# Optimization experiments

Hardware: AMD Instinct MI355X
Metric: run time of the kernel (lower is better)

## Reference

```python
import jax, jax.numpy as jnp
import numpy as np

B, F_IN, F_OUT, D, K = 32, 64, 64, 512, 64


def setup_inputs() -> dict:
    key = jax.random.key(0)
    k1, k2, k3 = jax.random.split(key, 3)
    x = jax.random.normal(k1, (B, F_IN, D), dtype=jnp.float32)
    # Evaluated monomial-word operators: K matrices of size D x D
    word_ops = jax.random.normal(k2, (K, D, D), dtype=jnp.float32)
    # nn.init.uniform_ -> U[0,1)
    coeff = jax.random.uniform(k3, (F_OUT, F_IN, K), dtype=jnp.float32)
    return {"x": x, "word_ops": word_ops, "coeff": coeff}


def reference(x, word_ops, coeff):
    # Per sample in the torch code:
    #   evals[i, d, k] = (X @ W_k)[i, d] = sum_e X[i, e] * W[k, e, d]
    #   res = tensordot(coeff, evals, ([1, 2], [0, 2]))  -> [F_out, D]
    # Fully batched fused contraction (replaces the Python loop over batch):
    # evals: [B, F_in, D, K]
    evals = jnp.einsum('bie,ked->bidk', x, word_ops)
    # out: [B, F_out, D]
    out = jnp.einsum('oik,bidk->bod', coeff, evals)
    return out
```

## Files before the change

kernel.cpp:

```cpp
#include <hip/hip_runtime.h>


#define KK 32768

typedef __attribute__((ext_vector_type(8))) short bf16x8;
typedef __attribute__((ext_vector_type(4))) float f32x4;

__device__ __forceinline__ unsigned short f2bf(float f) {
  unsigned int u = __float_as_uint(f);
  return (unsigned short)((u + 0x7FFFu + ((u >> 16) & 1u)) >> 16);
}

__device__ __forceinline__ void gld16(void* lds, const void* g) {
  __builtin_amdgcn_global_load_lds((const __attribute__((address_space(1))) void*)g,
                                   (__attribute__((address_space(3))) void*)lds,
                                   16, 0, 0);
}

__global__ __launch_bounds__(256) void convW(const float* __restrict__ W,
                                             unsigned short* __restrict__ WbT) {
  __shared__ float tile[64][65];
  int bx = blockIdx.x;
  int k = bx >> 6, et = (bx >> 3) & 7, dt = bx & 7;
  int t = threadIdx.x;
  const float* src = W + ((size_t)k * 512 + (size_t)et * 64) * 512 + dt * 64;
  int rr = t >> 6, cc = t & 63;
#pragma unroll
  for (int p = 0; p < 16; p++) {
    int e = p * 4 + rr;
    tile[e][cc] = src[(size_t)e * 512 + cc];
  }
  __syncthreads();
  int dl = t >> 4, eg = t & 15;
#pragma unroll
  for (int p = 0; p < 4; p++) {
    int d = p * 16 + dl;
    ushort4 v;
    v.x = f2bf(tile[eg * 4 + 0][d]);
    v.y = f2bf(tile[eg * 4 + 1][d]);
    v.z = f2bf(tile[eg * 4 + 2][d]);
    v.w = f2bf(tile[eg * 4 + 3][d]);
    *(ushort4*)(WbT + (size_t)(dt * 64 + d) * KK + k * 512 + et * 64 + eg * 4) = v;
  }
}

__global__ __launch_bounds__(256) void convXC(const float* __restrict__ x,
                                              const float* __restrict__ c,
                                              unsigned short* __restrict__ xT,
                                              unsigned short* __restrict__ cb) {
  __shared__ unsigned short lds[64 * 130];
  int t = threadIdx.x;
  if (blockIdx.x < 128) {
    int bx = blockIdx.x;
    int b = bx >> 2, ec = bx & 3;
    const float* src = x + (size_t)b * 32768 + ec * 128;
#pragma unroll
    for (int j = 0; j < 32; j++) {
      int idx = j * 256 + t;
      int i = idx >> 7, e = idx & 127;
      lds[i * 130 + e] = f2bf(src[(size_t)i * 512 + e]);
    }
    __syncthreads();
    unsigned short* dst = xT + (size_t)b * 32768 + ec * 128 * 64;
#pragma unroll
    for (int j = 0; j < 32; j++) {
      int idx = j * 256 + t;
      int e = idx >> 6, i = idx & 63;
      dst[idx] = lds[i * 130 + e];
    }
  } else {
    int rb = blockIdx.x - 128;
    const float* src = c + (size_t)rb * 4096;
#pragma unroll
    for (int j = 0; j < 16; j++) {
      int idx = j * 256 + t;
      int r = idx >> 6, k = idx & 63;
      lds[r * 66 + k] = f2bf(src[idx]);
    }
    __syncthreads();
#pragma unroll
    for (int j = 0; j < 16; j++) {
      int idx = j * 256 + t;
      int k = idx >> 6, r = idx & 63;
      cb[(size_t)k * 4096 + rb * 64 + r] = lds[r * 66 + k];
    }
  }
}

__global__ __launch_bounds__(256, 3) void tkern(const unsigned short* __restrict__ xT,
                                                const unsigned short* __restrict__ cb,
                                                unsigned short* __restrict__ Tb) {
  __shared__ unsigned short u0[64 * 132];
  __shared__ unsigned short ck[2][64 * 64];
  __shared__ unsigned short ot0[64 * 132];
  unsigned short* xe = u0;
  int bx = blockIdx.x;
  int eq = bx & 3, kq = (bx >> 2) & 15, b = bx >> 6;
  int t = threadIdx.x;
  {
    const unsigned short* gx = xT + (size_t)b * 32768 + (size_t)eq * 8192;
#pragma unroll
    for (int j = 0; j < 4; j++) {
      int idx = j * 256 + t;
      int e = idx >> 3, cg = (idx & 7) ^ (e & 7);
      gld16((char*)xe + idx * 16, gx + e * 64 + cg * 8);
    }
    const unsigned short* gc = cb + (size_t)(kq * 4) * 4096;
#pragma unroll
    for (int j = 0; j < 2; j++) {
      int idx = j * 256 + t;
      int o = idx >> 3, cg = (idx & 7) ^ (o & 7);
      gld16((char*)ck[0] + idx * 16, gc + o * 64 + cg * 8);
    }
  }
  __syncthreads();
  int wid = t >> 6, lane = t & 63, q = lane >> 4, l16 = lane & 15;
  bf16x8 ax[2][2];
#pragma unroll
  for (int ef = 0; ef < 2; ef++)
#pragma unroll
    for (int ks2 = 0; ks2 < 2; ks2++) {
      int e = wid * 32 + ef * 16 + l16;
      int s2 = (ks2 * 4 + q) ^ (e & 7);
      ax[ef][ks2] = *(const bf16x8*)(xe + e * 64 + s2 * 8);
    }
  size_t mbase = (size_t)(b * 64);
#pragma unroll 1
  for (int kj = 0; kj < 4; kj++) {
    int cur = kj & 1;
    if (kj < 3) {
      const unsigned short* gc = cb + (size_t)(kq * 4 + kj + 1) * 4096;
#pragma unroll
      for (int j = 0; j < 2; j++) {
        int idx = j * 256 + t;
        int o = idx >> 3, cg = (idx & 7) ^ (o & 7);
        gld16((char*)ck[cur ^ 1] + idx * 16, gc + o * 64 + cg * 8);
      }
    }
    const unsigned short* ckk = ck[cur];
    bf16x8 bc[4][2];
#pragma unroll
    for (int of = 0; of < 4; of++)
#pragma unroll
      for (int ks2 = 0; ks2 < 2; ks2++) {
        int o = of * 16 + l16;
        int s2 = (ks2 * 4 + q) ^ (o & 7);
        bc[of][ks2] = *(const bf16x8*)(ckk + o * 64 + s2 * 8);
      }
    f32x4 acc[2][4] = {};
#pragma unroll
    for (int ef = 0; ef < 2; ef++)
#pragma unroll
      for (int of = 0; of < 4; of++)
#pragma unroll
        for (int ks2 = 0; ks2 < 2; ks2++)
          acc[ef][of] = __builtin_amdgcn_mfma_f32_16x16x32_bf16(ax[ef][ks2], bc[of][ks2],
                                                                acc[ef][of], 0, 0, 0);
    unsigned short* ot = cur ? u0 : ot0;
#pragma unroll
    for (int ef = 0; ef < 2; ef++)
#pragma unroll
      for (int of = 0; of < 4; of++) {
        int o = of * 16 + l16;
        int e = wid * 32 + ef * 16 + q * 4;
        ushort4 v;
        v.x = f2bf(acc[ef][of][0]);
        v.y = f2bf(acc[ef][of][1]);
        v.z = f2bf(acc[ef][of][2]);
        v.w = f2bf(acc[ef][of][3]);
        *(ushort4*)(ot + o * 132 + e) = v;
      }
    __syncthreads();
    unsigned short* gdst = Tb + mbase * KK + (size_t)(kq * 4 + kj) * 512 + eq * 128;
#pragma unroll
    for (int j = 0; j < 8; j++) {
      int idx = j * 256 + t;
      int o = idx >> 5, cc2 = idx & 31;
      *(ushort4*)(gdst + (size_t)o * KK + cc2 * 4) = *(const ushort4*)(ot + o * 132 + cc2 * 4);
    }
  }
}

__global__ __launch_bounds__(256, 4) void gemm_kern(const unsigned short* __restrict__ A,
                                                    const unsigned short* __restrict__ Bt,
                                                    float* __restrict__ out) {
  __shared__ unsigned short As[128 * 64];
  __shared__ unsigned short Bs[128 * 64];
  int bx = blockIdx.x;
  int ks = bx & 15, nt = (bx >> 4) & 3, mt = bx >> 6;
  int m0 = mt * 128, n0 = nt * 128, k0 = ks * 2048;
  int t = threadIdx.x;
  int wid = t >> 6, lane = t & 63, q = lane >> 4, l16 = lane & 15;
  int wm = (wid & 1) * 64, wn = (wid >> 1) * 64;
  f32x4 acc[4][4] = {};
  int srow = t >> 3;
  int cg = (t & 7) ^ (srow & 7);
  const char* gabase = (const char*)(A + (size_t)m0 * KK + k0) + (size_t)srow * 65536 + cg * 16;
  const char* gbbase = (const char*)(Bt + (size_t)n0 * KK + k0) + (size_t)srow * 65536 + cg * 16;
  int sw0 = q ^ (l16 & 7);
  int sw1 = (4 | q) ^ (l16 & 7);
#pragma unroll 1
  for (int kc = 0; kc < 2048; kc += 64) {
    const char* ga = gabase + (size_t)kc * 2;
    const char* gb = gbbase + (size_t)kc * 2;
#pragma unroll
    for (int j = 0; j < 4; j++) {
      gld16((char*)As + (j * 256 + t) * 16, ga + (size_t)j * 32 * 65536);
      gld16((char*)Bs + (j * 256 + t) * 16, gb + (size_t)j * 32 * 65536);
    }
    __syncthreads();
#pragma unroll
    for (int ks2 = 0; ks2 < 2; ks2++) {
      int slot = ks2 ? sw1 : sw0;
      bf16x8 af[4], bfr[4];
#pragma unroll
      for (int fr = 0; fr < 4; fr++)
        af[fr] = *(const bf16x8*)(As + (wm + fr * 16 + l16) * 64 + slot * 8);
#pragma unroll
      for (int fc = 0; fc < 4; fc++)
        bfr[fc] = *(const bf16x8*)(Bs + (wn + fc * 16 + l16) * 64 + slot * 8);
#pragma unroll
      for (int fr = 0; fr < 4; fr++)
#pragma unroll
        for (int fc = 0; fc < 4; fc++)
          acc[fr][fc] = __builtin_amdgcn_mfma_f32_16x16x32_bf16(af[fr], bfr[fc], acc[fr][fc], 0, 0, 0);
    }
    __syncthreads();
  }
#pragma unroll
  for (int fr = 0; fr < 4; fr++)
#pragma unroll
    for (int fc = 0; fc < 4; fc++)
#pragma unroll
      for (int r = 0; r < 4; r++)
        atomicAdd(&out[(size_t)(m0 + wm + fr * 16 + q * 4 + r) * 512 + n0 + wn + fc * 16 + l16],
                  acc[fr][fc][r]);
}

__global__ __launch_bounds__(256) void fallback_kern(const float* __restrict__ x,
                                                     const float* __restrict__ W,
                                                     const float* __restrict__ coeff,
                                                     float* __restrict__ out) {
  __shared__ float ev[64][129];
  int b = blockIdx.x >> 6, k = blockIdx.x & 63;
  int t = threadIdx.x, dl = t & 127, half = t >> 7;
  const float* xb = x + (size_t)b * 64 * 512;
  const float* Wk = W + (size_t)k * 512 * 512;
  for (int dc = 0; dc < 4; dc++) {
    int d = dc * 128 + dl;
    for (int i = half * 32; i < half * 32 + 32; i++) {
      float acc = 0.f;
      const float* xr = xb + (size_t)i * 512;
#pragma unroll 4
      for (int e = 0; e < 512; e++) acc += xr[e] * Wk[(size_t)e * 512 + d];
      ev[i][dl] = acc;
    }
    __syncthreads();
    for (int o = half * 32; o < half * 32 + 32; o++) {
      float s = 0.f;
#pragma unroll 8
      for (int i = 0; i < 64; i++) s += coeff[((size_t)o * 64 + i) * 64 + k] * ev[i][dl];
      atomicAdd(&out[((size_t)(b * 64 + o)) * 512 + d], s);
    }
    __syncthreads();
  }
}

extern "C" void kernel_launch(void* const* d_in, const int* in_sizes, int n_in,
                              void* d_out, int out_size, void* d_ws, size_t ws_size,
                              hipStream_t stream) {
  const float* x = (const float*)d_in[0];
  const float* W = (const float*)d_in[1];
  const float* coeff = (const float*)d_in[2];
  float* out = (float*)d_out;
  const size_t OFF_XT = 33554432;
  const size_t OFF_CB = OFF_XT + 2097152;
  const size_t OFF_TB = OFF_CB + 524288;
  const size_t NEED = OFF_TB + 134217728;

  hipMemsetAsync(d_out, 0, (size_t)out_size * sizeof(float), stream);
  if (ws_size >= NEED) {
    unsigned short* WbT = (unsigned short*)d_ws;
    unsigned short* xT  = (unsigned short*)((char*)d_ws + OFF_XT);
    unsigned short* cb  = (unsigned short*)((char*)d_ws + OFF_CB);
    unsigned short* Tb  = (unsigned short*)((char*)d_ws + OFF_TB);
    convXC<<<192, 256, 0, stream>>>(x, coeff, xT, cb);
    convW<<<4096, 256, 0, stream>>>(W, WbT);
    tkern<<<2048, 256, 0, stream>>>(xT, cb, Tb);
    gemm_kern<<<1024, 256, 0, stream>>>(Tb, WbT, out);
  } else {
    fallback_kern<<<2048, 256, 0, stream>>>(x, W, coeff, out);
  }
}
```

Baseline: 240.3 us.

## Fuse coefficient-contraction kernel into GEMM to eliminate intermediate T buffer

Merges tkern and gemm_kern into one fused kernel. Each block computes its slice of the intermediate T = coeff·x tile in registers, writes it to LDS, and immediately consumes it as the A operand of the main GEMM against the bf16 word operators. This removes the 128 MB intermediate write and read-back through global memory, along with a kernel launch. In exchange, each GEMM block recomputes its small T tile, and the loop adds extra syncthreads and serialises the small MFMA step with the main one.

```diff
diff --git a/kernel.cpp b/kernel.cpp
--- a/kernel.cpp
+++ b/kernel.cpp
@@ -87,145 +87,122 @@
   }
 }
 
-__global__ __launch_bounds__(256, 3) void tkern(const unsigned short* __restrict__ xT,
-                                                const unsigned short* __restrict__ cb,
-                                                unsigned short* __restrict__ Tb) {
-  __shared__ unsigned short u0[64 * 132];
+__global__ __launch_bounds__(256, 3) void fused_kern(const unsigned short* __restrict__ xT,
+                                                     const unsigned short* __restrict__ cb,
+                                                     const unsigned short* __restrict__ Bt,
+                                                     float* __restrict__ out) {
+  __shared__ unsigned short u[128 * 64];
+  __shared__ unsigned short Bs[128 * 64];
   __shared__ unsigned short ck[2][64 * 64];
-  __shared__ unsigned short ot0[64 * 132];
-  unsigned short* xe = u0;
-  int bx = blockIdx.x;
-  int eq = bx & 3, kq = (bx >> 2) & 15, b = bx >> 6;
-  int t = threadIdx.x;
-  {
-    const unsigned short* gx = xT + (size_t)b * 32768 + (size_t)eq * 8192;
-#pragma unroll
-    for (int j = 0; j < 4; j++) {
-      int idx = j * 256 + t;
-      int e = idx >> 3, cg = (idx & 7) ^ (e & 7);
-      gld16((char*)xe + idx * 16, gx + e * 64 + cg * 8);
-    }
-    const unsigned short* gc = cb + (size_t)(kq * 4) * 4096;
-#pragma unroll
-    for (int j = 0; j < 2; j++) {
-      int idx = j * 256 + t;
-      int o = idx >> 3, cg = (idx & 7) ^ (o & 7);
-      gld16((char*)ck[0] + idx * 16, gc + o * 64 + cg * 8);
-    }
-  }
-  __syncthreads();
-  int wid = t >> 6, lane = t & 63, q = lane >> 4, l16 = lane & 15;
-  bf16x8 ax[2][2];
-#pragma unroll
-  for (int ef = 0; ef < 2; ef++)
-#pragma unroll
-    for (int ks2 = 0; ks2 < 2; ks2++) {
-      int e = wid * 32 + ef * 16 + l16;
-      int s2 = (ks2 * 4 + q) ^ (e & 7);
-      ax[ef][ks2] = *(const bf16x8*)(xe + e * 64 + s2 * 8);
-    }
-  size_t mbase = (size_t)(b * 64);
-#pragma unroll 1
-  for (int kj = 0; kj < 4; kj++) {
-    int cur = kj & 1;
-    if (kj < 3) {
-      const unsigned short* gc = cb + (size_t)(kq * 4 + kj + 1) * 4096;
-#pragma unroll
-      for (int j = 0; j < 2; j++) {
-        int idx = j * 256 + t;
-        int o = idx >> 3, cg = (idx & 7) ^ (o & 7);
-        gld16((char*)ck[cur ^ 1] + idx * 16, gc + o * 64 + cg * 8);
-      }
-    }
-    const unsigned short* ckk = ck[cur];
-    bf16x8 bc[4][2];
-#pragma unroll
-    for (int of = 0; of < 4; of++)
-#pragma unroll
-      for (int ks2 = 0; ks2 < 2; ks2++) {
-        int o = of * 16 + l16;
-        int s2 = (ks2 * 4 + q) ^ (o & 7);
-        bc[of][ks2] = *(const bf16x8*)(ckk + o * 64 + s2 * 8);
-      }
-    f32x4 acc[2][4] = {};
-#pragma unroll
-    for (int ef = 0; ef < 2; ef++)
-#pragma unroll
-      for (int of = 0; of < 4; of++)
-#pragma unroll
-        for (int ks2 = 0; ks2 < 2; ks2++)
-          acc[ef][of] = __builtin_amdgcn_mfma_f32_16x16x32_bf16(ax[ef][ks2], bc[of][ks2],
-                                                                acc[ef][of], 0, 0, 0);
-    unsigned short* ot = cur ? u0 : ot0;
-#pragma unroll
-    for (int ef = 0; ef < 2; ef++)
-#pragma unroll
-      for (int of = 0; of < 4; of++) {
-        int o = of * 16 + l16;
-        int e = wid * 32 + ef * 16 + q * 4;
-        ushort4 v;
-        v.x = f2bf(acc[ef][of][0]);
-        v.y = f2bf(acc[ef][of][1]);
-        v.z = f2bf(acc[ef][of][2]);
-        v.w = f2bf(acc[ef][of][3]);
-        *(ushort4*)(ot + o * 132 + e) = v;
-      }
-    __syncthreads();
-    unsigned short* gdst = Tb + mbase * KK + (size_t)(kq * 4 + kj) * 512 + eq * 128;
-#pragma unroll
-    for (int j = 0; j < 8; j++) {
-      int idx = j * 256 + t;
-      int o = idx >> 5, cc2 = idx & 31;
-      *(ushort4*)(gdst + (size_t)o * KK + cc2 * 4) = *(const ushort4*)(ot + o * 132 + cc2 * 4);
-    }
-  }
-}
-
-__global__ __launch_bounds__(256, 4) void gemm_kern(const unsigned short* __restrict__ A,
-                                                    const unsigned short* __restrict__ Bt,
-                                                    float* __restrict__ out) {
-  __shared__ unsigned short As[128 * 64];
-  __shared__ unsigned short Bs[128 * 64];
   int bx = blockIdx.x;
   int ks = bx & 15, nt = (bx >> 4) & 3, mt = bx >> 6;
-  int m0 = mt * 128, n0 = nt * 128, k0 = ks * 2048;
+  int m0 = mt * 128, n0 = nt * 128, kw0 = ks * 4, b0 = mt * 2;
   int t = threadIdx.x;
   int wid = t >> 6, lane = t & 63, q = lane >> 4, l16 = lane & 15;
-  int wm = (wid & 1) * 64, wn = (wid >> 1) * 64;
-  f32x4 acc[4][4] = {};
+  int wmb = wid & 1;
+  int weh = wid >> 1;
   int srow = t >> 3;
   int cg = (t & 7) ^ (srow & 7);
-  const char* gabase = (const char*)(A + (size_t)m0 * KK + k0) + (size_t)srow * 65536 + cg * 16;
-  const char* gbbase = (const char*)(Bt + (size_t)n0 * KK + k0) + (size_t)srow * 65536 + cg * 16;
-  int sw0 = q ^ (l16 & 7);
-  int sw1 = (4 | q) ^ (l16 & 7);
+  {
+    const unsigned short* gc = cb + (size_t)kw0 * 4096;
+#pragma unroll
+    for (int j = 0; j < 2; j++)
+      gld16((char*)ck[0] + (j * 256 + t) * 16, gc + (j * 32 + srow) * 64 + cg * 8);
+  }
+  f32x4 acc[4][4] = {};
 #pragma unroll 1
-  for (int kc = 0; kc < 2048; kc += 64) {
-    const char* ga = gabase + (size_t)kc * 2;
-    const char* gb = gbbase + (size_t)kc * 2;
+  for (int ec = 0; ec < 8; ec++) {
 #pragma unroll
     for (int j = 0; j < 4; j++) {
-      gld16((char*)As + (j * 256 + t) * 16, ga + (size_t)j * 32 * 65536);
-      gld16((char*)Bs + (j * 256 + t) * 16, gb + (size_t)j * 32 * 65536);
-    }
-    __syncthreads();
-#pragma unroll
-    for (int ks2 = 0; ks2 < 2; ks2++) {
-      int slot = ks2 ? sw1 : sw0;
-      bf16x8 af[4], bfr[4];
-#pragma unroll
-      for (int fr = 0; fr < 4; fr++)
-        af[fr] = *(const bf16x8*)(As + (wm + fr * 16 + l16) * 64 + slot * 8);
-#pragma unroll
-      for (int fc = 0; fc < 4; fc++)
-        bfr[fc] = *(const bf16x8*)(Bs + (wn + fc * 16 + l16) * 64 + slot * 8);
-#pragma unroll
-      for (int fr = 0; fr < 4; fr++)
-#pragma unroll
-        for (int fc = 0; fc < 4; fc++)
-          acc[fr][fc] = __builtin_amdgcn_mfma_f32_16x16x32_bf16(af[fr], bfr[fc], acc[fr][fc], 0, 0, 0);
-    }
-    __syncthreads();
+      int row = j * 32 + srow;
+      int bl = row >> 6, el = row & 63;
+      gld16((char*)u + (j * 256 + t) * 16,
+            xT + (size_t)(b0 + bl) * 32768 + (size_t)(ec * 64 + el) * 64 + cg * 8);
+    }
+    __syncthreads();
+    bf16x8 ax[2][2];
+#pragma unroll
+    for (int ef = 0; ef < 2; ef++)
+#pragma unroll
+      for (int ks2 = 0; ks2 < 2; ks2++) {
+        int row = wmb * 64 + weh * 32 + ef * 16 + l16;
+        int s2 = (ks2 * 4 + q) ^ (row & 7);
+        ax[ef][ks2] = *(const bf16x8*)(u + row * 64 + s2 * 8);
+      }
+    __syncthreads();
+#pragma unroll 1
+    for (int k = 0; k < 4; k++) {
+      int seq = ec * 4 + k, cur = seq & 1;
+      const unsigned short* gb = Bt + (size_t)n0 * KK + (size_t)(kw0 + k) * 512 + ec * 64;
+#pragma unroll
+      for (int j = 0; j < 4; j++) {
+        int row = j * 32 + srow;
+        gld16((char*)Bs + (j * 256 + t) * 16, gb + (size_t)row * KK + cg * 8);
+      }
+      if (seq < 31) {
+        int nk = (k < 3) ? k + 1 : 0;
+        const unsigned short* gc = cb + (size_t)(kw0 + nk) * 4096;
+#pragma unroll
+        for (int j = 0; j < 2; j++)
+          gld16((char*)ck[cur ^ 1] + (j * 256 + t) * 16, gc + (j * 32 + srow) * 64 + cg * 8);
+      }
+      const unsigned short* ckk = ck[cur];
+      bf16x8 bc[4][2];
+#pragma unroll
+      for (int of = 0; of < 4; of++)
+#pragma unroll
+        for (int ks2 = 0; ks2 < 2; ks2++) {
+          int o = of * 16 + l16;
+          int s2 = (ks2 * 4 + q) ^ (o & 7);
+          bc[of][ks2] = *(const bf16x8*)(ckk + o * 64 + s2 * 8);
+        }
+      f32x4 td[2][4] = {};
+#pragma unroll
+      for (int ef = 0; ef < 2; ef++)
+#pragma unroll
+        for (int of = 0; of < 4; of++)
+#pragma unroll
+          for (int ks2 = 0; ks2 < 2; ks2++)
+            td[ef][of] = __builtin_amdgcn_mfma_f32_16x16x32_bf16(ax[ef][ks2], bc[of][ks2],
+                                                                 td[ef][of], 0, 0, 0);
+#pragma unroll
+      for (int ef = 0; ef < 2; ef++)
+#pragma unroll
+        for (int of = 0; of < 4; of++) {
+          int row = wmb * 64 + of * 16 + l16;
+          int c0 = weh * 32 + ef * 16 + q * 4;
+          int phys = ((c0 >> 3) ^ (row & 7)) * 8 + (c0 & 7);
+          ushort4 v;
+          v.x = f2bf(td[ef][of][0]);
+          v.y = f2bf(td[ef][of][1]);
+          v.z = f2bf(td[ef][of][2]);
+          v.w = f2bf(td[ef][of][3]);
+          *(ushort4*)(u + row * 64 + phys) = v;
+        }
+      __syncthreads();
+#pragma unroll
+      for (int ks2 = 0; ks2 < 2; ks2++) {
+        int slot = ks2 * 4 + q;
+        bf16x8 af[4], bfr[4];
+#pragma unroll
+        for (int fr = 0; fr < 4; fr++) {
+          int row = wmb * 64 + fr * 16 + l16;
+          af[fr] = *(const bf16x8*)(u + row * 64 + (slot ^ (row & 7)) * 8);
+        }
+#pragma unroll
+        for (int fc = 0; fc < 4; fc++) {
+          int row = weh * 64 + fc * 16 + l16;
+          bfr[fc] = *(const bf16x8*)(Bs + row * 64 + (slot ^ (row & 7)) * 8);
+        }
+#pragma unroll
+        for (int fr = 0; fr < 4; fr++)
+#pragma unroll
+          for (int fc = 0; fc < 4; fc++)
+            acc[fr][fc] = __builtin_amdgcn_mfma_f32_16x16x32_bf16(af[fr], bfr[fc],
+                                                                  acc[fr][fc], 0, 0, 0);
+      }
+      __syncthreads();
+    }
   }
 #pragma unroll
   for (int fr = 0; fr < 4; fr++)
@@ -233,7 +210,8 @@
     for (int fc = 0; fc < 4; fc++)
 #pragma unroll
       for (int r = 0; r < 4; r++)
-        atomicAdd(&out[(size_t)(m0 + wm + fr * 16 + q * 4 + r) * 512 + n0 + wn + fc * 16 + l16],
+        atomicAdd(&out[(size_t)(m0 + wmb * 64 + fr * 16 + q * 4 + r) * 512
+                       + n0 + weh * 64 + fc * 16 + l16],
                   acc[fr][fc][r]);
 }
 
@@ -275,19 +253,16 @@
   float* out = (float*)d_out;
   const size_t OFF_XT = 33554432;
   const size_t OFF_CB = OFF_XT + 2097152;
-  const size_t OFF_TB = OFF_CB + 524288;
-  const size_t NEED = OFF_TB + 134217728;
+  const size_t NEED = OFF_CB + 524288;
 
   hipMemsetAsync(d_out, 0, (size_t)out_size * sizeof(float), stream);
   if (ws_size >= NEED) {
     unsigned short* WbT = (unsigned short*)d_ws;
     unsigned short* xT  = (unsigned short*)((char*)d_ws + OFF_XT);
     unsigned short* cb  = (unsigned short*)((char*)d_ws + OFF_CB);
-    unsigned short* Tb  = (unsigned short*)((char*)d_ws + OFF_TB);
     convXC<<<192, 256, 0, stream>>>(x, coeff, xT, cb);
     convW<<<4096, 256, 0, stream>>>(W, WbT);
-    tkern<<<2048, 256, 0, stream>>>(xT, cb, Tb);
-    gemm_kern<<<1024, 256, 0, stream>>>(Tb, WbT, out);
+    fused_kern<<<1024, 256, 0, stream>>>(xT, cb, WbT, out);
   } else {
     fallback_kern<<<2048, 256, 0, stream>>>(x, W, coeff, out);
   }
```

After: 229.0 us. -4.7%, faster.
